# Performance work log

Hardware: AMD Instinct MI355X
Metric: run time of the kernel (lower is better)

Reference implementation:

```python
import jax, jax.numpy as jnp
import numpy as np

B, T, D = 16, 2048, 64
K = 8192


def setup_inputs() -> dict:
    key = jax.random.key(0)
    k_x, k_cb = jax.random.split(key)
    x = jax.random.normal(k_x, (B, T, D), dtype=jnp.float32)
    # codebook initialized as randn(K, D) / sqrt(D), as in EMAQuantizer.__init__
    codebook = jax.random.normal(k_cb, (K, D), dtype=jnp.float32) / jnp.sqrt(jnp.float32(D))
    return {"x": x, "codebook": codebook}


def reference(x, codebook):
    """EMAQuantizer.forward (eval mode): nearest-codebook lookup + straight-through.

    x: [B, T, D], codebook: [K, D] -> (x_q_st [B,T,D], indices [B,T])
    """
    orig_shape = x.shape
    x_flat = x.reshape(-1, x.shape[-1])                       # [N, D]
    x2 = jnp.sum(x_flat * x_flat, axis=1, keepdims=True)      # [N, 1]
    e2 = jnp.sum(codebook * codebook, axis=1)[None, :]        # [1, K]
    xe = x_flat @ codebook.T                                  # [N, K]
    dist = x2 + e2 - 2.0 * xe                                 # [N, K] squared L2
    indices = jnp.argmin(dist, axis=1)                        # [N]
    x_q = codebook[indices].reshape(orig_shape)               # gather lookup
    x_q_st = x + jax.lax.stop_gradient(x_q - x)               # straight-through
    return x_q_st, indices.reshape(orig_shape[:-1])
```

## Files before the change

### kernel.cpp

```cpp
#include <hip/hip_runtime.h>
#include <hip/hip_bf16.h>
#include <math.h>

#define N_ROWS 32768
#define KCODES 8192
#define DDIM 64

typedef __attribute__((ext_vector_type(8))) short bf16x8;
typedef __attribute__((ext_vector_type(4))) float f32x4;

#define CAP 16
#define O_XBF   0
#define O_QPERM 4194304UL
#define O_X2    5242880UL
#define O_E2    5373952UL
#define O_E2MAX 5406720UL
#define O_CNT   5406736UL
#define O_GMIN  5537808UL
#define O_SLOTS 5668880UL
#define WS_NEEDED (O_SLOTS + (size_t)N_ROWS * CAP * 4)

__device__ __forceinline__ unsigned short f2bf(float f) {
    __hip_bfloat16 h = __float2bfloat16(f);
    union { __hip_bfloat16 b; unsigned short u; } u;
    u.b = h;
    return u.u;
}

__device__ __forceinline__ float bf2f(unsigned short u) {
    return __uint_as_float(((unsigned int)u) << 16);
}

__global__ __launch_bounds__(256) void prep_kernel(const float* __restrict__ x,
                                                   const float* __restrict__ cb,
                                                   unsigned short* __restrict__ xbf,
                                                   uint4* __restrict__ qperm,
                                                   float* __restrict__ x2,
                                                   float* __restrict__ e2,
                                                   int* __restrict__ e2max_bits,
                                                   int* __restrict__ cnt) {
#pragma clang fp contract(off)
    int t = blockIdx.x * 256 + threadIdx.x;
    bool iscb = (t >= N_ROWS);
    int r = iscb ? (t - N_ROWS) : t;
    const float* src = iscb ? (cb + (size_t)r * DDIM) : (x + (size_t)r * DDIM);
    if (!iscb) {
        cnt[r] = 0;
    }

    uint4 ch[8];
#pragma unroll
    for (int h = 0; h < 8; ++h) {
        float4 v0 = ((const float4*)src)[h * 2];
        float4 v1 = ((const float4*)src)[h * 2 + 1];
        ushort4 a, b;
        a.x = f2bf(v0.x); a.y = f2bf(v0.y); a.z = f2bf(v0.z); a.w = f2bf(v0.w);
        b.x = f2bf(v1.x); b.y = f2bf(v1.y); b.z = f2bf(v1.z); b.w = f2bf(v1.w);
        union { struct { ushort4 lo, hi; } s; uint4 u; } pk;
        pk.s.lo = a; pk.s.hi = b;
        ch[h] = pk.u;
    }
    if (!iscb) {
        uint4* dst = (uint4*)(xbf + (size_t)r * DDIM);
#pragma unroll
        for (int h = 0; h < 8; ++h) dst[h] = ch[h];
    } else {
        int g = r >> 4, l15 = r & 15;
#pragma unroll
        for (int h = 0; h < 8; ++h) {
            int slot = (g * 2 + (h >> 2)) * 64 + (h & 3) * 16 + l15;
            qperm[slot] = ch[h];
        }
    }

    float acc[8];
#pragma unroll
    for (int j = 0; j < 8; ++j) { float v = src[j]; acc[j] = v * v; }
#pragma unroll
    for (int i = 8; i < 64; i += 8)
#pragma unroll
        for (int j = 0; j < 8; ++j) { float v = src[i + j]; acc[j] = acc[j] + v * v; }
    float s = ((acc[0] + acc[1]) + (acc[2] + acc[3])) + ((acc[4] + acc[5]) + (acc[6] + acc[7]));
    if (!iscb) {
        x2[r] = s;
    } else {
        e2[r] = s;
        float wm = s;
#pragma unroll
        for (int m = 1; m < 64; m <<= 1) wm = fmaxf(wm, __shfl_xor(wm, m, 64));
        if ((threadIdx.x & 63) == 0) atomicMax(e2max_bits, __float_as_int(wm));
    }
}

__global__ __launch_bounds__(512) void screen_fused_kernel(
    const unsigned short* __restrict__ xbf, const uint4* __restrict__ qperm,
    const float* __restrict__ x2g, const float* __restrict__ e2g,
    const int* __restrict__ e2max_bits,
    int* __restrict__ cnt, int* __restrict__ slots) {
    __shared__ float tilemax_lds[64 * 64];
    __shared__ unsigned short xs_lds[64][64];
    __shared__ unsigned int wl[4096];
    __shared__ float thr_lds[64];
    __shared__ int wcnt;

    const int tid = threadIdx.x;
    const int w = tid >> 6;
    const int lane = tid & 63;
    const int l15 = lane & 15;
    const int quad = lane >> 4;
    const int row0 = blockIdx.x * 64;
    const int T0 = w * 64;

    ((uint4*)xs_lds)[tid] = *((const uint4*)(xbf + (size_t)row0 * DDIM) + tid);
    if (tid == 0) wcnt = 0;

    bf16x8 afrag[4][2];
#pragma unroll
    for (int rt = 0; rt < 4; ++rt)
#pragma unroll
        for (int s = 0; s < 2; ++s)
            afrag[rt][s] = *(const bf16x8*)(xbf + (size_t)(row0 + rt * 16 + l15) * DDIM +
                                            s * 32 + quad * 8);

    const uint4* pB = qperm + (size_t)T0 * 128 + lane;
    const float* pE = e2g + T0 * 16 + l15;

    bf16x8 b0[2], b1[2];
    float ee2[2];
#pragma unroll
    for (int i = 0; i < 2; ++i) {
        b0[i] = *(const bf16x8*)(pB + (size_t)i * 128);
        b1[i] = *(const bf16x8*)(pB + (size_t)i * 128 + 64);
        ee2[i] = pE[i * 16];
    }

    float tmax[4][4];
#pragma unroll
    for (int rt = 0; rt < 4; ++rt)
#pragma unroll
        for (int reg = 0; reg < 4; ++reg) tmax[rt][reg] = -3.0e38f;

    for (int g = 0; g < 8; ++g) {
#pragma unroll 2
        for (int j = 0; j < 8; ++j) {
            const int t = g * 8 + j;
            const int buf = t & 1;
            const bf16x8 B0 = b0[buf];
            const bf16x8 B1 = b1[buf];
            const float eh = -0.5f * ee2[buf];
            if (t < 62) {
                const uint4* p = pB + (size_t)(t + 2) * 128;
                b0[buf] = *(const bf16x8*)p;
                b1[buf] = *(const bf16x8*)(p + 64);
                ee2[buf] = pE[(t + 2) * 16];
            }
            const f32x4 cin = {eh, eh, eh, eh};
#pragma unroll
            for (int rt = 0; rt < 4; ++rt) {
                f32x4 acc = __builtin_amdgcn_mfma_f32_16x16x32_bf16(afrag[rt][0], B0, cin, 0, 0, 0);
                acc = __builtin_amdgcn_mfma_f32_16x16x32_bf16(afrag[rt][1], B1, acc, 0, 0, 0);
#pragma unroll
                for (int reg = 0; reg < 4; ++reg)
                    tmax[rt][reg] = fmaxf(tmax[rt][reg], acc[reg]);
            }
        }
        const int gidx = w * 8 + g;
#pragma unroll
        for (int rt = 0; rt < 4; ++rt)
#pragma unroll
            for (int reg = 0; reg < 4; ++reg) {
                float v = tmax[rt][reg];
                v = fmaxf(v, __shfl_xor(v, 1, 64));
                v = fmaxf(v, __shfl_xor(v, 2, 64));
                v = fmaxf(v, __shfl_xor(v, 4, 64));
                v = fmaxf(v, __shfl_xor(v, 8, 64));
                if (l15 == 0) tilemax_lds[gidx * 64 + rt * 16 + quad * 4 + reg] = v;
                tmax[rt][reg] = -3.0e38f;
            }
    }
    __syncthreads();

    if (tid < 64) {
        float gs = -3.0e38f;
        for (int e = 0; e < 64; ++e) gs = fmaxf(gs, tilemax_lds[e * 64 + tid]);
        const float e2max = __int_as_float(*e2max_bits);
        thr_lds[tid] = gs - 0.005f * sqrtf(x2g[row0 + tid] * e2max) - 0.01f;
    }
    __syncthreads();

    for (int idx = tid; idx < 4096; idx += 512) {
        if (tilemax_lds[idx] >= thr_lds[idx & 63]) {
            int pos = atomicAdd(&wcnt, 1);
            wl[pos] = (unsigned int)idx;
        }
    }
    __syncthreads();

    const int nwl = wcnt;
    for (int p = w; p < nwl; p += 8) {
        const unsigned int e = wl[p];
        const int r = (int)(e & 63u);
        const int g = (int)(e >> 6);
        const float thr_r = thr_lds[r];
        const int row = row0 + r;
#pragma unroll
        for (int half = 0; half < 2; ++half) {
            const int c = g * 128 + half * 64 + lane;
            float s = -0.5f * e2g[c];
            const int cg = c >> 4, cl = c & 15;
#pragma unroll
            for (int h = 0; h < 8; ++h) {
                const int slot = (cg * 2 + (h >> 2)) * 64 + (h & 3) * 16 + cl;
                union { uint4 u; unsigned short us[8]; } qd, xd;
                qd.u = qperm[slot];
                xd.u = *(const uint4*)&xs_lds[r][h * 8];
#pragma unroll
                for (int k = 0; k < 8; ++k)
                    s = fmaf(bf2f(xd.us[k]), bf2f(qd.us[k]), s);
            }
            if (s >= thr_r) {
                int pos = atomicAdd(&cnt[row], 1);
                if (pos < CAP) slots[(size_t)row * CAP + pos] = c;
            }
        }
    }
}

__global__ __launch_bounds__(256) void finalize2_kernel(const float* __restrict__ x,
                                                        const float* __restrict__ cb,
                                                        const float* __restrict__ x2,
                                                        const float* __restrict__ e2,
                                                        const int* __restrict__ cnt,
                                                        const int* __restrict__ slots,
                                                        float* __restrict__ out) {
    __shared__ float bvs[256];
    __shared__ int bis[256];
    int t = blockIdx.x * 256 + threadIdx.x;
    int r = t >> 2, j = t & 3;
    const int tid = threadIdx.x;

    float xr[64];
#pragma unroll
    for (int q = 0; q < 16; ++q) {
        float4 v = ((const float4*)(x + (size_t)r * DDIM))[q];
        xr[q * 4 + 0] = v.x; xr[q * 4 + 1] = v.y; xr[q * 4 + 2] = v.z; xr[q * 4 + 3] = v.w;
    }
    float x2v = x2[r];

    float bv = 3.0e38f;
    int bi = 0x7fffffff;
    int c = cnt[r];
    if (c > 0 && c <= CAP) {
        for (int i = j; i < c; i += 4) {
            int code = slots[(size_t)r * CAP + i];
            float xe = 0.0f;
            const float4* e4 = (const float4*)(cb + (size_t)code * DDIM);
#pragma unroll
            for (int q = 0; q < 16; ++q) {
                float4 ev = e4[q];
                xe = fmaf(xr[q * 4 + 0], ev.x, xe);
                xe = fmaf(xr[q * 4 + 1], ev.y, xe);
                xe = fmaf(xr[q * 4 + 2], ev.z, xe);
                xe = fmaf(xr[q * 4 + 3], ev.w, xe);
            }
            float ts = x2v + e2[code];
            float dist = fmaf(-2.0f, xe, ts);
            if (dist < bv || (dist == bv && code < bi)) { bv = dist; bi = code; }
        }
    } else {
        for (int code = j; code < KCODES; code += 4) {
            float xe = 0.0f;
            const float4* e4 = (const float4*)(cb + (size_t)code * DDIM);
#pragma unroll
            for (int q = 0; q < 16; ++q) {
                float4 ev = e4[q];
                xe = fmaf(xr[q * 4 + 0], ev.x, xe);
                xe = fmaf(xr[q * 4 + 1], ev.y, xe);
                xe = fmaf(xr[q * 4 + 2], ev.z, xe);
                xe = fmaf(xr[q * 4 + 3], ev.w, xe);
            }
            float ts = x2v + e2[code];
            float dist = fmaf(-2.0f, xe, ts);
            if (dist < bv || (dist == bv && code < bi)) { bv = dist; bi = code; }
        }
    }
    bvs[tid] = bv;
    bis[tid] = bi;
    __syncthreads();
    int base = tid & ~3;
    if (j == 0) {
#pragma unroll
        for (int jj = 1; jj < 4; ++jj) {
            float v = bvs[base + jj];
            int ii = bis[base + jj];
            if (v < bv || (v == bv && ii < bi)) { bv = v; bi = ii; }
        }
        bis[base] = bi;
    }
    __syncthreads();
    int best = bis[base];

    const float4* qs = (const float4*)(cb + (size_t)best * DDIM);
    float4* os = (float4*)(out + (size_t)r * DDIM);
#pragma unroll
    for (int i = 0; i < 4; ++i) {
        float4 qv = qs[j * 4 + i];
        float xv0 = xr[(j * 4 + i) * 4 + 0], xv1 = xr[(j * 4 + i) * 4 + 1];
        float xv2 = xr[(j * 4 + i) * 4 + 2], xv3 = xr[(j * 4 + i) * 4 + 3];
        float4 ov;
        ov.x = xv0 + (qv.x - xv0);
        ov.y = xv1 + (qv.y - xv1);
        ov.z = xv2 + (qv.z - xv2);
        ov.w = xv3 + (qv.w - xv3);
        os[j * 4 + i] = ov;
    }
    if (j == 0) out[(size_t)N_ROWS * DDIM + r] = (float)best;
}

#define SPLITK 4
#define KPER (KCODES / SPLITK)
#define TM 128
#define TKT 128
#define NTILES (KPER / TKT)
#define LDSX 132
#define LDSE 132

__global__ __launch_bounds__(256) void sumsq_kernel(const float* __restrict__ x,
                                                    const float* __restrict__ cb,
                                                    float* __restrict__ ws) {
#pragma clang fp contract(off)
    int t = blockIdx.x * 256 + threadIdx.x;
    const float* src;
    float* dst;
    if (t < KCODES) { src = cb + (size_t)t * DDIM; dst = ws + t; }
    else { int r = t - KCODES; src = x + (size_t)r * DDIM; dst = ws + KCODES + r; }
    float acc[8];
#pragma unroll
    for (int j = 0; j < 8; ++j) { float v = src[j]; acc[j] = v * v; }
#pragma unroll
    for (int i = 8; i < 64; i += 8)
#pragma unroll
        for (int j = 0; j < 8; ++j) { float v = src[i + j]; acc[j] = acc[j] + v * v; }
    *dst = ((acc[0] + acc[1]) + (acc[2] + acc[3])) + ((acc[4] + acc[5]) + (acc[6] + acc[7]));
}

__global__ __launch_bounds__(256) void dist_argmin_kernel(const float* __restrict__ x,
                                                          const float* __restrict__ cb,
                                                          const float* __restrict__ e2g,
                                                          const float* __restrict__ x2g,
                                                          float2* __restrict__ partial) {
    __shared__ float smem[DDIM * LDSX + DDIM * LDSE];
    float* Xs = smem;
    float* Es = smem + DDIM * LDSX;
    const int tid = threadIdx.x;
    const int row0 = blockIdx.x * TM;
    const int code0 = blockIdx.y * KPER;
    const int tr = tid >> 4, tc = tid & 15;
    for (int i = tid; i < TM * 16; i += 256) {
        int r = i >> 4, q = i & 15;
        float4 v = ((const float4*)(x + (size_t)(row0 + r) * DDIM))[q];
        Xs[(4 * q + 0) * LDSX + r] = v.x; Xs[(4 * q + 1) * LDSX + r] = v.y;
        Xs[(4 * q + 2) * LDSX + r] = v.z; Xs[(4 * q + 3) * LDSX + r] = v.w;
    }
    float x2v[8];
#pragma unroll
    for (int j = 0; j < 8; ++j) x2v[j] = x2g[row0 + tr * 8 + j];
    float bestV[8]; int bestI[8];
#pragma unroll
    for (int j = 0; j < 8; ++j) { bestV[j] = 3.0e38f; bestI[j] = 0; }
    for (int t = 0; t < NTILES; ++t) {
        __syncthreads();
        const int cbase = code0 + t * TKT;
        for (int i = tid; i < TKT * 16; i += 256) {
            int c = i >> 4, q = i & 15;
            float4 v = ((const float4*)(cb + (size_t)(cbase + c) * DDIM))[q];
            Es[(4 * q + 0) * LDSE + c] = v.x; Es[(4 * q + 1) * LDSE + c] = v.y;
            Es[(4 * q + 2) * LDSE + c] = v.z; Es[(4 * q + 3) * LDSE + c] = v.w;
        }
        __syncthreads();
        float acc[8][8];
#pragma unroll
        for (int a = 0; a < 8; ++a)
#pragma unroll
            for (int b = 0; b < 8; ++b) acc[a][b] = 0.0f;
#pragma unroll 4
        for (int d = 0; d < DDIM; ++d) {
            float xv[8], ev[8];
            float4 xa = *(const float4*)&Xs[d * LDSX + tr * 8];
            float4 xb = *(const float4*)&Xs[d * LDSX + tr * 8 + 4];
            float4 ea = *(const float4*)&Es[d * LDSE + tc * 8];
            float4 eb = *(const float4*)&Es[d * LDSE + tc * 8 + 4];
            xv[0] = xa.x; xv[1] = xa.y; xv[2] = xa.z; xv[3] = xa.w;
            xv[4] = xb.x; xv[5] = xb.y; xv[6] = xb.z; xv[7] = xb.w;
            ev[0] = ea.x; ev[1] = ea.y; ev[2] = ea.z; ev[3] = ea.w;
            ev[4] = eb.x; ev[5] = eb.y; ev[6] = eb.z; ev[7] = eb.w;
#pragma unroll
            for (int a = 0; a < 8; ++a)
#pragma unroll
                for (int b = 0; b < 8; ++b) acc[a][b] = fmaf(xv[a], ev[b], acc[a][b]);
        }
#pragma unroll
        for (int b = 0; b < 8; ++b) {
            int ci = cbase + tc * 8 + b;
            float e2 = e2g[ci];
#pragma unroll
            for (int a = 0; a < 8; ++a) {
                float ts = x2v[a] + e2;
                float dist = fmaf(-2.0f, acc[a][b], ts);
                if (dist < bestV[a]) { bestV[a] = dist; bestI[a] = ci; }
            }
        }
    }
    __syncthreads();
    float* redV = Es;
    int* redI = (int*)(Es + TM * 16);
#pragma unroll
    for (int a = 0; a < 8; ++a) {
        redV[(tr * 8 + a) * 16 + tc] = bestV[a];
        redI[(tr * 8 + a) * 16 + tc] = bestI[a];
    }
    __syncthreads();
    if (tid < TM) {
        float bv = redV[tid * 16];
        int bi = redI[tid * 16];
#pragma unroll
        for (int c = 1; c < 16; ++c) {
            float v = redV[tid * 16 + c];
            int ii = redI[tid * 16 + c];
            if (v < bv || (v == bv && ii < bi)) { bv = v; bi = ii; }
        }
        partial[(size_t)(row0 + tid) * SPLITK + blockIdx.y] = make_float2(bv, __int_as_float(bi));
    }
}

__global__ __launch_bounds__(256) void finalize_kernel(const float2* __restrict__ partial,
                                                       const float* __restrict__ x,
                                                       const float* __restrict__ cb,
                                                       float* __restrict__ out) {
    int t = blockIdx.x * 256 + threadIdx.x;
    int r = t >> 2, j = t & 3;
    float2 p = partial[(size_t)r * SPLITK];
    float bv = p.x;
    int bi = __float_as_int(p.y);
#pragma unroll
    for (int k = 1; k < SPLITK; ++k) {
        float2 q = partial[(size_t)r * SPLITK + k];
        int qi = __float_as_int(q.y);
        if (q.x < bv || (q.x == bv && qi < bi)) { bv = q.x; bi = qi; }
    }
    const float4* xs = (const float4*)(x + (size_t)r * DDIM);
    const float4* qs = (const float4*)(cb + (size_t)bi * DDIM);
    float4* os = (float4*)(out + (size_t)r * DDIM);
#pragma unroll
    for (int i = 0; i < 4; ++i) {
        float4 xv = xs[j * 4 + i];
        float4 qv = qs[j * 4 + i];
        float4 ov;
        ov.x = xv.x + (qv.x - xv.x); ov.y = xv.y + (qv.y - xv.y);
        ov.z = xv.z + (qv.z - xv.z); ov.w = xv.w + (qv.w - xv.w);
        os[j * 4 + i] = ov;
    }
    if (j == 0) out[(size_t)N_ROWS * DDIM + r] = (float)bi;
}

extern "C" void kernel_launch(void* const* d_in, const int* in_sizes, int n_in,
                              void* d_out, int out_size, void* d_ws, size_t ws_size,
                              hipStream_t stream) {
    const float* x = (const float*)d_in[0];
    const float* cb = (const float*)d_in[1];
    float* out = (float*)d_out;

    if (ws_size >= WS_NEEDED) {
        unsigned char* ws = (unsigned char*)d_ws;
        unsigned short* xbf = (unsigned short*)(ws + O_XBF);
        uint4* qperm = (uint4*)(ws + O_QPERM);
        float* x2 = (float*)(ws + O_X2);
        float* e2 = (float*)(ws + O_E2);
        int* e2max_bits = (int*)(ws + O_E2MAX);
        int* cnt = (int*)(ws + O_CNT);
        int* slots = (int*)(ws + O_SLOTS);

        prep_kernel<<<(N_ROWS + KCODES) / 256, 256, 0, stream>>>(x, cb, xbf, qperm, x2, e2,
                                                                 e2max_bits, cnt);
        screen_fused_kernel<<<N_ROWS / 64, 512, 0, stream>>>(xbf, qperm, x2, e2, e2max_bits,
                                                             cnt, slots);
        finalize2_kernel<<<(N_ROWS * 4) / 256, 256, 0, stream>>>(x, cb, x2, e2, cnt, slots, out);
    } else {
        float* ws = (float*)d_ws;
        float* e2 = ws;
        float* x2 = ws + KCODES;
        float2* partial = (float2*)(ws + KCODES + N_ROWS);
        sumsq_kernel<<<(KCODES + N_ROWS) / 256, 256, 0, stream>>>(x, cb, ws);
        dim3 grid(N_ROWS / TM, SPLITK);
        dist_argmin_kernel<<<grid, 256, 0, stream>>>(x, cb, e2, x2, partial);
        finalize_kernel<<<(N_ROWS * 4) / 256, 256, 0, stream>>>(partial, x, cb, out);
    }
}
```

Baseline: 163.4 us.

## Fuse candidate rescoring and output into screening kernel via LDS slots

The per-row candidate count and slot list move from global memory with global atomics into shared memory inside the screening kernel. The separate finalize kernel is removed: after a barrier, each group of 8 lanes rescores one row's candidates in fp32, reduces with shuffles and writes the straight-through output and index. This drops one kernel launch, the global cnt/slot traffic and the per-row counter reset in prep. In exchange it adds LDS pressure, which may lower occupancy, and the fallback full scan over all codes now runs inside the screening block.

New measurement: 143.5 us. 1.14x faster.

```diff
diff --git a/kernel.cpp b/kernel.cpp
--- a/kernel.cpp
+++ b/kernel.cpp
@@ -9,16 +9,14 @@
 typedef __attribute__((ext_vector_type(8))) short bf16x8;
 typedef __attribute__((ext_vector_type(4))) float f32x4;
 
-#define CAP 16
 #define O_XBF   0
 #define O_QPERM 4194304UL
 #define O_X2    5242880UL
 #define O_E2    5373952UL
 #define O_E2MAX 5406720UL
-#define O_CNT   5406736UL
-#define O_GMIN  5537808UL
 #define O_SLOTS 5668880UL
-#define WS_NEEDED (O_SLOTS + (size_t)N_ROWS * CAP * 4)
+#define WS_NEEDED (O_SLOTS + (size_t)N_ROWS * 16 * 4)
+#define CAPL 32
 
 __device__ __forceinline__ unsigned short f2bf(float f) {
     __hip_bfloat16 h = __float2bfloat16(f);
@@ -37,16 +35,12 @@
                                                    uint4* __restrict__ qperm,
                                                    float* __restrict__ x2,
                                                    float* __restrict__ e2,
-                                                   int* __restrict__ e2max_bits,
-                                                   int* __restrict__ cnt) {
+                                                   int* __restrict__ e2max_bits) {
 #pragma clang fp contract(off)
     int t = blockIdx.x * 256 + threadIdx.x;
     bool iscb = (t >= N_ROWS);
     int r = iscb ? (t - N_ROWS) : t;
     const float* src = iscb ? (cb + (size_t)r * DDIM) : (x + (size_t)r * DDIM);
-    if (!iscb) {
-        cnt[r] = 0;
-    }
 
     uint4 ch[8];
 #pragma unroll
@@ -94,13 +88,15 @@
 
 __global__ __launch_bounds__(512) void screen_fused_kernel(
     const unsigned short* __restrict__ xbf, const uint4* __restrict__ qperm,
+    const float* __restrict__ xg, const float* __restrict__ cbg,
     const float* __restrict__ x2g, const float* __restrict__ e2g,
-    const int* __restrict__ e2max_bits,
-    int* __restrict__ cnt, int* __restrict__ slots) {
+    const int* __restrict__ e2max_bits, float* __restrict__ out) {
     __shared__ float tilemax_lds[64 * 64];
     __shared__ unsigned short xs_lds[64][64];
     __shared__ unsigned int wl[4096];
     __shared__ float thr_lds[64];
+    __shared__ int cnt_lds[64];
+    __shared__ int slots_lds[64][CAPL];
     __shared__ int wcnt;
 
     const int tid = threadIdx.x;
@@ -113,6 +109,7 @@
 
     ((uint4*)xs_lds)[tid] = *((const uint4*)(xbf + (size_t)row0 * DDIM) + tid);
     if (tid == 0) wcnt = 0;
+    if (tid < 64) cnt_lds[tid] = 0;
 
     bf16x8 afrag[4][2];
 #pragma unroll
@@ -202,10 +199,9 @@
         const int r = (int)(e & 63u);
         const int g = (int)(e >> 6);
         const float thr_r = thr_lds[r];
-        const int row = row0 + r;
-#pragma unroll
-        for (int half = 0; half < 2; ++half) {
-            const int c = g * 128 + half * 64 + lane;
+#pragma unroll
+        for (int hh = 0; hh < 2; ++hh) {
+            const int c = g * 128 + hh * 64 + lane;
             float s = -0.5f * e2g[c];
             const int cg = c >> 4, cl = c & 15;
 #pragma unroll
@@ -219,102 +215,81 @@
                     s = fmaf(bf2f(xd.us[k]), bf2f(qd.us[k]), s);
             }
             if (s >= thr_r) {
-                int pos = atomicAdd(&cnt[row], 1);
-                if (pos < CAP) slots[(size_t)row * CAP + pos] = c;
-            }
-        }
-    }
-}
-
-__global__ __launch_bounds__(256) void finalize2_kernel(const float* __restrict__ x,
-                                                        const float* __restrict__ cb,
-                                                        const float* __restrict__ x2,
-                                                        const float* __restrict__ e2,
-                                                        const int* __restrict__ cnt,
-                                                        const int* __restrict__ slots,
-                                                        float* __restrict__ out) {
-    __shared__ float bvs[256];
-    __shared__ int bis[256];
-    int t = blockIdx.x * 256 + threadIdx.x;
-    int r = t >> 2, j = t & 3;
-    const int tid = threadIdx.x;
-
-    float xr[64];
-#pragma unroll
-    for (int q = 0; q < 16; ++q) {
-        float4 v = ((const float4*)(x + (size_t)r * DDIM))[q];
-        xr[q * 4 + 0] = v.x; xr[q * 4 + 1] = v.y; xr[q * 4 + 2] = v.z; xr[q * 4 + 3] = v.w;
-    }
-    float x2v = x2[r];
+                int pos = atomicAdd(&cnt_lds[r], 1);
+                if (pos < CAPL) slots_lds[r][pos] = c;
+            }
+        }
+    }
+    __syncthreads();
+
+    const int sub = lane >> 3;
+    const int ln8 = lane & 7;
+    const int r = w * 8 + sub;
+    const int row = row0 + r;
+    const int c = cnt_lds[r];
+    const float x2v = x2g[row];
+    const float4* xv4 = (const float4*)(xg + (size_t)row * DDIM);
 
     float bv = 3.0e38f;
     int bi = 0x7fffffff;
-    int c = cnt[r];
-    if (c > 0 && c <= CAP) {
-        for (int i = j; i < c; i += 4) {
-            int code = slots[(size_t)r * CAP + i];
+    if (c <= CAPL) {
+        for (int i = ln8; i < c; i += 8) {
+            int code = slots_lds[r][i];
             float xe = 0.0f;
-            const float4* e4 = (const float4*)(cb + (size_t)code * DDIM);
+            const float4* e4 = (const float4*)(cbg + (size_t)code * DDIM);
 #pragma unroll
             for (int q = 0; q < 16; ++q) {
+                float4 xv = xv4[q];
                 float4 ev = e4[q];
-                xe = fmaf(xr[q * 4 + 0], ev.x, xe);
-                xe = fmaf(xr[q * 4 + 1], ev.y, xe);
-                xe = fmaf(xr[q * 4 + 2], ev.z, xe);
-                xe = fmaf(xr[q * 4 + 3], ev.w, xe);
-            }
-            float ts = x2v + e2[code];
+                xe = fmaf(xv.x, ev.x, xe);
+                xe = fmaf(xv.y, ev.y, xe);
+                xe = fmaf(xv.z, ev.z, xe);
+                xe = fmaf(xv.w, ev.w, xe);
+            }
+            float ts = x2v + e2g[code];
             float dist = fmaf(-2.0f, xe, ts);
             if (dist < bv || (dist == bv && code < bi)) { bv = dist; bi = code; }
         }
     } else {
-        for (int code = j; code < KCODES; code += 4) {
+        for (int code = ln8; code < KCODES; code += 8) {
             float xe = 0.0f;
-            const float4* e4 = (const float4*)(cb + (size_t)code * DDIM);
+            const float4* e4 = (const float4*)(cbg + (size_t)code * DDIM);
 #pragma unroll
             for (int q = 0; q < 16; ++q) {
+                float4 xv = xv4[q];
                 float4 ev = e4[q];
-                xe = fmaf(xr[q * 4 + 0], ev.x, xe);
-                xe = fmaf(xr[q * 4 + 1], ev.y, xe);
-                xe = fmaf(xr[q * 4 + 2], ev.z, xe);
-                xe = fmaf(xr[q * 4 + 3], ev.w, xe);
-            }
-            float ts = x2v + e2[code];
+                xe = fmaf(xv.x, ev.x, xe);
+                xe = fmaf(xv.y, ev.y, xe);
+                xe = fmaf(xv.z, ev.z, xe);
+                xe = fmaf(xv.w, ev.w, xe);
+            }
+            float ts = x2v + e2g[code];
             float dist = fmaf(-2.0f, xe, ts);
             if (dist < bv || (dist == bv && code < bi)) { bv = dist; bi = code; }
         }
     }
-    bvs[tid] = bv;
-    bis[tid] = bi;
-    __syncthreads();
-    int base = tid & ~3;
-    if (j == 0) {
-#pragma unroll
-        for (int jj = 1; jj < 4; ++jj) {
-            float v = bvs[base + jj];
-            int ii = bis[base + jj];
-            if (v < bv || (v == bv && ii < bi)) { bv = v; bi = ii; }
-        }
-        bis[base] = bi;
-    }
-    __syncthreads();
-    int best = bis[base];
-
-    const float4* qs = (const float4*)(cb + (size_t)best * DDIM);
-    float4* os = (float4*)(out + (size_t)r * DDIM);
-#pragma unroll
-    for (int i = 0; i < 4; ++i) {
-        float4 qv = qs[j * 4 + i];
-        float xv0 = xr[(j * 4 + i) * 4 + 0], xv1 = xr[(j * 4 + i) * 4 + 1];
-        float xv2 = xr[(j * 4 + i) * 4 + 2], xv3 = xr[(j * 4 + i) * 4 + 3];
-        float4 ov;
-        ov.x = xv0 + (qv.x - xv0);
-        ov.y = xv1 + (qv.y - xv1);
-        ov.z = xv2 + (qv.z - xv2);
-        ov.w = xv3 + (qv.w - xv3);
-        os[j * 4 + i] = ov;
-    }
-    if (j == 0) out[(size_t)N_ROWS * DDIM + r] = (float)best;
+#pragma unroll
+    for (int m = 1; m < 8; m <<= 1) {
+        float ov = __shfl_xor(bv, m, 64);
+        int oi = __shfl_xor(bi, m, 64);
+        if (ov < bv || (ov == bv && oi < bi)) { bv = ov; bi = oi; }
+    }
+    {
+        const float4* qs4 = (const float4*)(cbg + (size_t)bi * DDIM);
+        float4* os4 = (float4*)(out + (size_t)row * DDIM);
+#pragma unroll
+        for (int i = 0; i < 2; ++i) {
+            float4 xv = xv4[ln8 * 2 + i];
+            float4 qv = qs4[ln8 * 2 + i];
+            float4 ov;
+            ov.x = xv.x + (qv.x - xv.x);
+            ov.y = xv.y + (qv.y - xv.y);
+            ov.z = xv.z + (qv.z - xv.z);
+            ov.w = xv.w + (qv.w - xv.w);
+            os4[ln8 * 2 + i] = ov;
+        }
+        if (ln8 == 0) out[(size_t)N_ROWS * DDIM + row] = (float)bi;
+    }
 }
 
 #define SPLITK 4
@@ -477,14 +452,11 @@
         float* x2 = (float*)(ws + O_X2);
         float* e2 = (float*)(ws + O_E2);
         int* e2max_bits = (int*)(ws + O_E2MAX);
-        int* cnt = (int*)(ws + O_CNT);
-        int* slots = (int*)(ws + O_SLOTS);
 
         prep_kernel<<<(N_ROWS + KCODES) / 256, 256, 0, stream>>>(x, cb, xbf, qperm, x2, e2,
-                                                                 e2max_bits, cnt);
-        screen_fused_kernel<<<N_ROWS / 64, 512, 0, stream>>>(xbf, qperm, x2, e2, e2max_bits,
-                                                             cnt, slots);
-        finalize2_kernel<<<(N_ROWS * 4) / 256, 256, 0, stream>>>(x, cb, x2, e2, cnt, slots, out);
+                                                                 e2max_bits);
+        screen_fused_kernel<<<N_ROWS / 64, 512, 0, stream>>>(xbf, qperm, x, cb, x2, e2,
+                                                             e2max_bits, out);
     } else {
         float* ws = (float*)d_ws;
         float* e2 = ws;
```
